# Kernel tuning notes

Hardware: AMD Instinct MI355X
Metric: run time of the kernel (lower is better)

Reference implementation:

```python
import jax, jax.numpy as jnp
import numpy as np

B, C, N, GP = 8, 512, 4096, 4


def _phi(x):
    return jax.nn.relu(x) + 1.0


def _ln(x, g, b):
    # LayerNorm over last dim, eps=1e-6 (matches nn.LayerNorm(C, eps=1e-6))
    mu = x.mean(-1, keepdims=True)
    var = ((x - mu) ** 2).mean(-1, keepdims=True)
    return (x - mu) * jax.lax.rsqrt(var + 1e-6) * g + b


def _sdpa_linear(q, k, v):
    # q,k,v: [G,C,n]
    c = q.shape[1]
    kv = jnp.einsum('gcn,gdn->gcd', k, v) / jnp.sqrt(jnp.asarray(c, q.dtype))
    ksum = k.sum(-1)                                              # [G,C]
    z = 1.0 / (jnp.einsum('gcn,gc->gn', q, ksum)[:, None, :] + 1e-6)  # [G,1,n]
    y = jnp.einsum('gcn,gcd->gdn', q, kv)                         # [G,C,n]
    return y * z


def _ffn_ln(x_res, y, g1, b1, f1w, f1b, f2w, f2b, g2, b2):
    # residual + ln1 + FFN + relu(ln2); io layout [G,C,n]
    h = _ln((x_res + y).transpose(0, 2, 1), g1, b1)               # [G,n,C]
    h = h + jnp.einsum('gnf,cf->gnc', jax.nn.relu(jnp.einsum('gnc,fc->gnf', h, f1w) + f1b), f2w) + f2b
    return jax.nn.relu(_ln(h, g2, b2)).transpose(0, 2, 1)


def _sa_block(x, wqk, wv, wphi, g1, b1, f1w, f1b, f2w, f2b, g2, b2):
    # SA_Layer_Linear: q_conv.weight == k_conv.weight, so q == k
    n = x.shape[-1]
    q = _phi(jnp.einsum('dc,gcn->gdn', wqk, x))
    v = jnp.einsum('dc,gcn->gdn', wv, x)
    phix = jnp.einsum('dc,gcn->gdn', wphi, x)
    qg = q.mean(-1, keepdims=True)                                # [G,C,1]
    alpha = jax.nn.softmax((qg * q).sum(1, keepdims=True), axis=-1) * n  # [G,1,n]
    y = _sdpa_linear(q, q * alpha, v) * phix
    return _ffn_ln(x, y, g1, b1, f1w, f1b, f2w, f2b, g2, b2)


def _cross_block(x, bsz, gp, wq, wk, wv, wphi, g1, b1, f1w, f1b, f2w, f2b, g2, b2):
    # Cross_SA_Layer_Linear: first group attends to k/v from group 0, rest passthrough
    n = x.shape[-1]
    first, rest = x[:bsz], x[bsz:]
    q = _phi(jnp.einsum('dc,gcn->gdn', wq, rest))                 # [(gp-1)B,C,n]
    k0 = _phi(jnp.einsum('dc,gcn->gdn', wk, first))               # [B,C,n]
    v0 = jnp.einsum('dc,gcn->gdn', wv, first)
    phi_first = jnp.einsum('dc,gcn->gdn', wphi, first)
    phi_rest = jnp.einsum('dc,gcn->gdn', wphi, rest)
    k = jnp.tile(k0, (gp - 1, 1, 1))
    v = jnp.tile(v0, (gp - 1, 1, 1))
    qg = jnp.tile(k0.mean(-1, keepdims=True), (gp - 1, 1, 1))
    alpha = jax.nn.softmax((qg * k).sum(1, keepdims=True), axis=-1) * n
    y = _sdpa_linear(q, k * alpha, v) * phi_rest                  # [(gp-1)B,C,n]
    y_first = y.mean(0, keepdims=True) * phi_first                # [B,C,n] via broadcast
    out_first = _ffn_ln(first, y_first, g1, b1, f1w, f1b, f2w, f2b, g2, b2)
    return jnp.concatenate([out_first, rest], axis=0)


def reference(feat, tw_qk, tw_v, tw_phi, tg1, tb1, tf1w, tf1b, tf2w, tf2b, tg2, tb2,
              cw_q, cw_k, cw_v, cw_phi, cg1, cb1, cf1w, cf1b, cf2w, cf2b, cg2, cb2):
    bsz, c, n = feat.shape
    gp = GP
    ng = n // gp
    # interval grouping: group i picks points {i, i+gp, i+2gp, ...}; vstack -> groups stacked on batch
    gx = (feat.transpose(0, 2, 1).reshape(bsz, ng, gp, c)
          .transpose(2, 0, 1, 3).reshape(gp * bsz, ng, c).transpose(0, 2, 1))
    f = _sa_block(gx, tw_qk, tw_v, tw_phi, tg1, tb1, tf1w, tf1b, tf2w, tf2b, tg2, tb2)
    # regroup: cat along feature dim then view(B,N,C) == interleave back
    t = (f.transpose(0, 2, 1).reshape(gp, bsz, ng, c)
         .transpose(1, 2, 0, 3).reshape(bsz, n, c))
    # contiguous re-split for cross block: group i = points [i*ng:(i+1)*ng]
    gx2 = (t.reshape(bsz, gp, ng, c).transpose(1, 0, 2, 3)
           .reshape(gp * bsz, ng, c).transpose(0, 2, 1))
    f2 = _cross_block(gx2, bsz, gp, cw_q, cw_k, cw_v, cw_phi, cg1, cb1, cf1w, cf1b, cf2w, cf2b, cg2, cb2)
    # final ungroup: out[i] = concat_j f2[B*j+i] -> [B,C,N]
    out = (f2.transpose(0, 2, 1).reshape(gp, bsz, ng, c)
           .transpose(1, 0, 2, 3).reshape(bsz, n, c).transpose(0, 2, 1))
    return out


def setup_inputs() -> dict:
    key = jax.random.key(0)
    ks = jax.random.split(key, 12)
    s = 0.02
    F = 4 * C
    d = {}
    d['feat'] = jax.random.normal(ks[0], (B, C, N), jnp.float32)
    # SA_Layer_Linear (trans_block) params
    d['tw_qk'] = jax.random.normal(ks[1], (C, C), jnp.float32) * s
    d['tw_v'] = jax.random.normal(ks[2], (C, C), jnp.float32) * s
    d['tw_phi'] = jax.random.normal(ks[3], (C, C), jnp.float32) * s
    d['tg1'] = jnp.ones((C,), jnp.float32)
    d['tb1'] = jnp.zeros((C,), jnp.float32)
    d['tf1w'] = jax.random.normal(ks[4], (F, C), jnp.float32) * s
    d['tf1b'] = jnp.zeros((F,), jnp.float32)
    d['tf2w'] = jax.random.normal(ks[5], (C, F), jnp.float32) * s
    d['tf2b'] = jnp.zeros((C,), jnp.float32)
    d['tg2'] = jnp.ones((C,), jnp.float32)
    d['tb2'] = jnp.zeros((C,), jnp.float32)
    # Cross_SA_Layer_Linear params
    d['cw_q'] = jax.random.normal(ks[6], (C, C), jnp.float32) * s
    d['cw_k'] = jax.random.normal(ks[7], (C, C), jnp.float32) * s
    d['cw_v'] = jax.random.normal(ks[8], (C, C), jnp.float32) * s
    d['cw_phi'] = jax.random.normal(ks[9], (C, C), jnp.float32) * s
    d['cg1'] = jnp.ones((C,), jnp.float32)
    d['cb1'] = jnp.zeros((C,), jnp.float32)
    d['cf1w'] = jax.random.normal(ks[10], (F, C), jnp.float32) * s
    d['cf1b'] = jnp.zeros((F,), jnp.float32)
    d['cf2w'] = jax.random.normal(ks[11], (C, F), jnp.float32) * s
    d['cf2b'] = jnp.zeros((C,), jnp.float32)
    d['cg2'] = jnp.ones((C,), jnp.float32)
    d['cb2'] = jnp.zeros((C,), jnp.float32)
    return d
```

## Files before the change

### kernel.cpp

```cpp
#include <hip/hip_runtime.h>
#include <math.h>

using u16 = unsigned short;
typedef __attribute__((ext_vector_type(8))) short short8;
typedef __attribute__((ext_vector_type(4))) float f32x4;

constexpr long kPLANE = 1024l * 512;
constexpr long SZW    = 512l * 512;
constexpr long MB     = 1l << 20;

__device__ __forceinline__ float bf2f(u16 u) {
  return __uint_as_float(((unsigned int)u) << 16);
}
__device__ __forceinline__ u16 f2bf(float f) {
  unsigned int x = __float_as_uint(f);
  x += 0x7fffu + ((x >> 16) & 1u);
  return (u16)(x >> 16);
}

__device__ __forceinline__ void lds_barrier() {
  asm volatile("s_waitcnt lgkmcnt(0)" ::: "memory");
  __builtin_amdgcn_s_barrier();
}

__global__ __launch_bounds__(256, 4) void gemm_mfma(
    const u16* __restrict__ A, long sA, int amask,
    const u16* __restrict__ B, long sB, int bmask,
    u16* __restrict__ Out, long sO,
    int M, int Nn, int K, float scale, int act,
    const float* __restrict__ bias,
    const float* __restrict__ rowscale, long sRS,
    const u16* __restrict__ pmul, const u16* __restrict__ resid)
{
  int gx = gridDim.x, gy = gridDim.y;
  int nwg = gx * gy * gridDim.z;
  int lin = blockIdx.x + gx * (blockIdx.y + gy * blockIdx.z);
  int qq = nwg >> 3, rr = nwg & 7;
  int xcd = lin & 7, idx = lin >> 3;
  int wg = (xcd < rr ? xcd * (qq + 1) : rr * (qq + 1) + (xcd - rr) * qq) + idx;
  int bx = wg % gx; int t_ = wg / gx; int by = t_ % gy; int g = t_ / gy;

  const u16* Ag = A + (long)(g & amask) * sA;
  const u16* Bg = B + (long)(g & bmask) * sB;
  u16* Og = Out + (long)g * sO;
  int m0 = by * 128, n0 = bx * 128;

  __shared__ __align__(16) u16 As[2][128 * 32];
  __shared__ __align__(16) u16 Bs[2][128 * 32];

  int tid = threadIdx.x;
  int w = tid >> 6, L = tid & 63;
  int wm = (w >> 1) * 64, wn = (w & 1) * 64;
  int l15 = L & 15, l4 = L >> 4;

  f32x4 acc[4][4] = {};

  int r0 = tid >> 2, r1 = r0 + 64;
  int kk = (tid & 3) * 8;
  int cxor = (tid >> 3) & 3;
  int s0 = r0 * 32 + (((tid & 3) ^ cxor) << 3);
  int s1 = s0 + 64 * 32;
  const u16* gA0 = Ag + (long)(m0 + r0) * K + kk;
  const u16* gA1 = Ag + (long)(m0 + r1) * K + kk;
  const u16* gB0 = Bg + (long)(n0 + r0) * K + kk;
  const u16* gB1 = Bg + (long)(n0 + r1) * K + kk;

  int rcol = (l4 << 3) ^ (((l15 >> 1) & 3) << 3);

  short8 ra0 = *(const short8*)gA0;
  short8 ra1 = *(const short8*)gA1;
  short8 rb0 = *(const short8*)gB0;
  short8 rb1 = *(const short8*)gB1;
  *(short8*)&As[0][s0] = ra0; *(short8*)&As[0][s1] = ra1;
  *(short8*)&Bs[0][s0] = rb0; *(short8*)&Bs[0][s1] = rb1;
  lds_barrier();

  int nsteps = K >> 5;
  for (int ks = 0; ks < nsteps; ++ks) {
    int cur = ks & 1;
    if (ks + 1 < nsteps) {
      int ko = (ks + 1) << 5;
      ra0 = *(const short8*)(gA0 + ko);
      ra1 = *(const short8*)(gA1 + ko);
      rb0 = *(const short8*)(gB0 + ko);
      rb1 = *(const short8*)(gB1 + ko);
    }
    short8 af[4], bf[4];
#pragma unroll
    for (int mi = 0; mi < 4; ++mi)
      af[mi] = *(const short8*)&As[cur][(wm + mi * 16 + l15) * 32 + rcol];
#pragma unroll
    for (int ni = 0; ni < 4; ++ni)
      bf[ni] = *(const short8*)&Bs[cur][(wn + ni * 16 + l15) * 32 + rcol];
#pragma unroll
    for (int mi = 0; mi < 4; ++mi)
#pragma unroll
      for (int ni = 0; ni < 4; ++ni)
        acc[mi][ni] = __builtin_amdgcn_mfma_f32_16x16x32_bf16(bf[ni], af[mi], acc[mi][ni], 0, 0, 0);
    if (ks + 1 < nsteps) {
      int nxt = cur ^ 1;
      *(short8*)&As[nxt][s0] = ra0; *(short8*)&As[nxt][s1] = ra1;
      *(short8*)&Bs[nxt][s0] = rb0; *(short8*)&Bs[nxt][s1] = rb1;
    }
    lds_barrier();
  }

#pragma unroll
  for (int mi = 0; mi < 4; ++mi) {
    int m = m0 + wm + mi * 16 + l15;
    float rs = rowscale ? rowscale[(long)g * sRS + m] : 1.f;
    float srs = scale * rs;
#pragma unroll
    for (int ni = 0; ni < 4; ++ni) {
      int nb = n0 + wn + ni * 16 + l4 * 4;
      long off = (long)m * Nn + nb;
      float v[4];
#pragma unroll
      for (int r = 0; r < 4; ++r) v[r] = acc[mi][ni][r] * srs;
      if (pmul) {
        ushort4 pm = *(const ushort4*)&pmul[(long)g * sO + off];
        v[0] *= bf2f(pm.x); v[1] *= bf2f(pm.y); v[2] *= bf2f(pm.z); v[3] *= bf2f(pm.w);
      }
      if (bias) {
        float4 bi = *(const float4*)&bias[nb];
        v[0] += bi.x; v[1] += bi.y; v[2] += bi.z; v[3] += bi.w;
      }
      if (resid) {
        ushort4 rd = *(const ushort4*)&resid[(long)g * sO + off];
        v[0] += bf2f(rd.x); v[1] += bf2f(rd.y); v[2] += bf2f(rd.z); v[3] += bf2f(rd.w);
      }
      if (act == 1) {
#pragma unroll
        for (int r = 0; r < 4; ++r) v[r] = fmaxf(v[r], 0.f);
      } else if (act == 2) {
#pragma unroll
        for (int r = 0; r < 4; ++r) v[r] = fmaxf(v[r], 0.f) + 1.f;
      }
      ushort4 o; o.x = f2bf(v[0]); o.y = f2bf(v[1]); o.z = f2bf(v[2]); o.w = f2bf(v[3]);
      *(ushort4*)&Og[off] = o;
    }
  }
}

__global__ __launch_bounds__(256) void cast7(
    const float* a0, const float* a1, const float* a2, const float* a3,
    const float* a4, const float* a5, const float* a6, u16* __restrict__ dst)
{
  int w = blockIdx.y;
  const float* s = w == 0 ? a0 : w == 1 ? a1 : w == 2 ? a2 : w == 3 ? a3
                 : w == 4 ? a4 : w == 5 ? a5 : a6;
  long i = (long)blockIdx.x * 256 + threadIdx.x;
  dst[(long)w * SZW + i] = f2bf(s[i]);
}

__global__ __launch_bounds__(256) void cast4(
    const float* a0, const float* a1, const float* a2, const float* a3,
    u16* __restrict__ dst)
{
  int w = blockIdx.y;
  const float* s = w == 0 ? a0 : w == 1 ? a1 : w == 2 ? a2 : a3;
  long i = (long)blockIdx.x * 256 + threadIdx.x;
  dst[(long)w * 1048576 + i] = f2bf(s[i]);
}

__global__ __launch_bounds__(256) void gather_feat(
    const float* __restrict__ feat, u16* __restrict__ gxT)
{
  __shared__ float t[32][132];
  int b = blockIdx.z, c0 = blockIdx.y * 32, nf0 = blockIdx.x * 128;
  int tx = threadIdx.x, ty = threadIdx.y;
  for (int r = ty; r < 32; r += 8)
    *(float4*)&t[r][tx * 4] = *(const float4*)&feat[((long)b * 512 + c0 + r) * 4096 + nf0 + tx * 4];
  __syncthreads();
  int n0o = nf0 >> 2;
  for (int gp = 0; gp < 4; ++gp) {
    long gbase = (long)(gp * 8 + b) * kPLANE;
    for (int jr = ty; jr < 32; jr += 8)
      gxT[gbase + (long)(n0o + jr) * 512 + c0 + tx] = f2bf(t[tx][jr * 4 + gp]);
  }
}

__global__ __launch_bounds__(256) void transpose_b(
    const u16* __restrict__ in, u16* __restrict__ out, const float* __restrict__ alpha)
{
  int g = blockIdx.z;
  const u16* I = in + (long)g * kPLANE;
  u16* O = out + (long)g * kPLANE;
  __shared__ u16 t[64][66];
  int n0 = blockIdx.x * 64, c0 = blockIdx.y * 64;
  int tx = threadIdx.x, ty = threadIdx.y;
  for (int r = ty; r < 64; r += 8)
    *(ushort2*)&t[r][tx * 2] = *(const ushort2*)&I[(long)(n0 + r) * 512 + c0 + tx * 2];
  __syncthreads();
  float al0 = 1.f, al1 = 1.f;
  if (alpha) {
    al0 = alpha[(long)g * 1024 + n0 + tx * 2];
    al1 = alpha[(long)g * 1024 + n0 + tx * 2 + 1];
  }
  for (int r = ty; r < 64; r += 8) {
    ushort2 wv;
    wv.x = f2bf(bf2f(t[tx * 2][r]) * al0);
    wv.y = f2bf(bf2f(t[tx * 2 + 1][r]) * al1);
    *(ushort2*)&O[(long)(c0 + r) * 1024 + n0 + tx * 2] = wv;
  }
}

__global__ __launch_bounds__(256) void colsum1(
    const u16* __restrict__ X, long sX, const float* __restrict__ alpha,
    float* __restrict__ part)
{
  int g = blockIdx.z, ch = blockIdx.y;
  int c = blockIdx.x * 256 + threadIdx.x;
  const u16* Xg = X + (long)g * sX;
  int nb = ch * 128;
  float s = 0.f;
  for (int i = 0; i < 128; ++i) {
    int n = nb + i;
    s += bf2f(Xg[(long)n * 512 + c]) * (alpha ? alpha[(long)g * 1024 + n] : 1.f);
  }
  part[(long)(g * 8 + ch) * 512 + c] = s;
}

__global__ __launch_bounds__(256) void colsum2(
    const float* __restrict__ part, float* __restrict__ out, float scale)
{
  int g = blockIdx.y;
  int c = blockIdx.x * 256 + threadIdx.x;
  float s = 0.f;
#pragma unroll
  for (int ch = 0; ch < 8; ++ch) s += part[(long)(g * 8 + ch) * 512 + c];
  out[(long)g * 512 + c] = s * scale;
}

__global__ __launch_bounds__(256) void rowdot(
    const u16* __restrict__ X, long sX, const float* __restrict__ w, int wmask,
    float* __restrict__ out, int mode)
{
  int g = blockIdx.y;
  int n = blockIdx.x * 4 + (threadIdx.x >> 6);
  int L = threadIdx.x & 63;
  const u16* row = X + (long)g * sX + (long)n * 512;
  short8 xv = *(const short8*)&row[L * 8];
  const float* wg = w + (long)(g & wmask) * 512;
  float4 w0 = *(const float4*)&wg[L * 8];
  float4 w1 = *(const float4*)&wg[L * 8 + 4];
  float s = bf2f((u16)xv[0]) * w0.x + bf2f((u16)xv[1]) * w0.y +
            bf2f((u16)xv[2]) * w0.z + bf2f((u16)xv[3]) * w0.w +
            bf2f((u16)xv[4]) * w1.x + bf2f((u16)xv[5]) * w1.y +
            bf2f((u16)xv[6]) * w1.z + bf2f((u16)xv[7]) * w1.w;
#pragma unroll
  for (int off = 32; off >= 1; off >>= 1) s += __shfl_down(s, off);
  if (L == 0) out[(long)g * 1024 + n] = mode ? 1.f / (s + 1e-6f) : s;
}

__global__ __launch_bounds__(256) void softmax_row(
    const float* __restrict__ sc, float* __restrict__ out)
{
  int g = blockIdx.x, tid = threadIdx.x;
  const float* s = sc + (long)g * 1024;
  float* o = out + (long)g * 1024;
  __shared__ float red[256];
  float lm = -3.4e38f;
  for (int n = tid; n < 1024; n += 256) lm = fmaxf(lm, s[n]);
  red[tid] = lm; __syncthreads();
  for (int st = 128; st; st >>= 1) { if (tid < st) red[tid] = fmaxf(red[tid], red[tid + st]); __syncthreads(); }
  float mx = red[0]; __syncthreads();
  float ls = 0.f;
  for (int n = tid; n < 1024; n += 256) ls += __expf(s[n] - mx);
  red[tid] = ls; __syncthreads();
  for (int st = 128; st; st >>= 1) { if (tid < st) red[tid] += red[tid + st]; __syncthreads(); }
  float inv = 1024.f / red[0];
  for (int n = tid; n < 1024; n += 256) o[n] = __expf(s[n] - mx) * inv;
}

__global__ __launch_bounds__(256) void ln_rows(
    const u16* __restrict__ X, const float* __restrict__ gamma,
    const float* __restrict__ beta, u16* __restrict__ Out, int relu)
{
  long m = (long)blockIdx.x * 4 + (threadIdx.x >> 6);
  int L = threadIdx.x & 63;
  const u16* x = X + m * 512;
  u16* o = Out + m * 512;
  short8 xv = *(const short8*)&x[L * 8];
  float v[8];
#pragma unroll
  for (int j = 0; j < 8; ++j) v[j] = bf2f((u16)xv[j]);
  float s = v[0] + v[1] + v[2] + v[3] + v[4] + v[5] + v[6] + v[7];
#pragma unroll
  for (int off = 32; off >= 1; off >>= 1) s += __shfl_xor(s, off);
  float mu = s * (1.f / 512.f);
  float ss = 0.f;
#pragma unroll
  for (int j = 0; j < 8; ++j) { v[j] -= mu; ss += v[j] * v[j]; }
#pragma unroll
  for (int off = 32; off >= 1; off >>= 1) ss += __shfl_xor(ss, off);
  float rs = rsqrtf(ss * (1.f / 512.f) + 1e-6f);
  float4 g0 = *(const float4*)&gamma[L * 8];
  float4 g1 = *(const float4*)&gamma[L * 8 + 4];
  float4 b0 = *(const float4*)&beta[L * 8];
  float4 b1 = *(const float4*)&beta[L * 8 + 4];
  float ov[8];
  ov[0] = v[0] * rs * g0.x + b0.x; ov[1] = v[1] * rs * g0.y + b0.y;
  ov[2] = v[2] * rs * g0.z + b0.z; ov[3] = v[3] * rs * g0.w + b0.w;
  ov[4] = v[4] * rs * g1.x + b1.x; ov[5] = v[5] * rs * g1.y + b1.y;
  ov[6] = v[6] * rs * g1.z + b1.z; ov[7] = v[7] * rs * g1.w + b1.w;
  if (relu) {
#pragma unroll
    for (int j = 0; j < 8; ++j) ov[j] = fmaxf(ov[j], 0.f);
  }
  short8 r;
#pragma unroll
  for (int j = 0; j < 8; ++j) r[j] = (short)f2bf(ov[j]);
  *(short8*)&o[L * 8] = r;
}

__global__ __launch_bounds__(256) void ln_gather(
    const u16* __restrict__ X, const float* __restrict__ gamma,
    const float* __restrict__ beta, u16* __restrict__ Out)
{
  long bid = (long)blockIdx.x * 4 + (threadIdx.x >> 6);
  int L = threadIdx.x & 63;
  int g2 = (int)(bid >> 10), m = (int)(bid & 1023);
  long src = ((long)((m & 3) * 8 + (g2 & 7)) * 1024 + (g2 >> 3) * 256 + (m >> 2)) * 512;
  const u16* x = X + src;
  u16* o = Out + bid * 512;
  short8 xv = *(const short8*)&x[L * 8];
  float v[8];
#pragma unroll
  for (int j = 0; j < 8; ++j) v[j] = bf2f((u16)xv[j]);
  float s = v[0] + v[1] + v[2] + v[3] + v[4] + v[5] + v[6] + v[7];
#pragma unroll
  for (int off = 32; off >= 1; off >>= 1) s += __shfl_xor(s, off);
  float mu = s * (1.f / 512.f);
  float ss = 0.f;
#pragma unroll
  for (int j = 0; j < 8; ++j) { v[j] -= mu; ss += v[j] * v[j]; }
#pragma unroll
  for (int off = 32; off >= 1; off >>= 1) ss += __shfl_xor(ss, off);
  float rs = rsqrtf(ss * (1.f / 512.f) + 1e-6f);
  float4 g0 = *(const float4*)&gamma[L * 8];
  float4 g1 = *(const float4*)&gamma[L * 8 + 4];
  float4 b0 = *(const float4*)&beta[L * 8];
  float4 b1 = *(const float4*)&beta[L * 8 + 4];
  float ov[8];
  ov[0] = v[0] * rs * g0.x + b0.x; ov[1] = v[1] * rs * g0.y + b0.y;
  ov[2] = v[2] * rs * g0.z + b0.z; ov[3] = v[3] * rs * g0.w + b0.w;
  ov[4] = v[4] * rs * g1.x + b1.x; ov[5] = v[5] * rs * g1.y + b1.y;
  ov[6] = v[6] * rs * g1.z + b1.z; ov[7] = v[7] * rs * g1.w + b1.w;
  short8 r;
#pragma unroll
  for (int j = 0; j < 8; ++j) r[j] = (short)f2bf(fmaxf(ov[j], 0.f));
  *(short8*)&o[L * 8] = r;
}

__global__ __launch_bounds__(256) void ybar_k(
    const u16* __restrict__ Y, float* __restrict__ yb)
{
  long idx = ((long)blockIdx.x * 256 + threadIdx.x) * 2;
  float s0 = 0.f, s1 = 0.f;
#pragma unroll
  for (int g = 0; g < 24; ++g) {
    ushort2 u = *(const ushort2*)&Y[(long)g * kPLANE + idx];
    s0 += bf2f(u.x); s1 += bf2f(u.y);
  }
  float2 o; o.x = s0 * (1.f / 24.f); o.y = s1 * (1.f / 24.f);
  *(float2*)&yb[idx] = o;
}

__global__ __launch_bounds__(256) void hfirst_ln(
    const u16* __restrict__ gx2, const u16* __restrict__ phiF,
    const float* __restrict__ yb, const float* __restrict__ gamma,
    const float* __restrict__ beta, u16* __restrict__ Out)
{
  long m = (long)blockIdx.x * 4 + (threadIdx.x >> 6);
  int L = threadIdx.x & 63;
  long off = m * 512 + L * 8;
  long yoff = (m & 1023) * 512 + L * 8;
  short8 a8 = *(const short8*)&gx2[off];
  short8 f8 = *(const short8*)&phiF[off];
  float4 y0 = *(const float4*)&yb[yoff];
  float4 y1 = *(const float4*)&yb[yoff + 4];
  float v[8];
  v[0] = bf2f((u16)a8[0]) + y0.x * bf2f((u16)f8[0]);
  v[1] = bf2f((u16)a8[1]) + y0.y * bf2f((u16)f8[1]);
  v[2] = bf2f((u16)a8[2]) + y0.z * bf2f((u16)f8[2]);
  v[3] = bf2f((u16)a8[3]) + y0.w * bf2f((u16)f8[3]);
  v[4] = bf2f((u16)a8[4]) + y1.x * bf2f((u16)f8[4]);
  v[5] = bf2f((u16)a8[5]) + y1.y * bf2f((u16)f8[5]);
  v[6] = bf2f((u16)a8[6]) + y1.z * bf2f((u16)f8[6]);
  v[7] = bf2f((u16)a8[7]) + y1.w * bf2f((u16)f8[7]);
  float s = v[0] + v[1] + v[2] + v[3] + v[4] + v[5] + v[6] + v[7];
#pragma unroll
  for (int off2 = 32; off2 >= 1; off2 >>= 1) s += __shfl_xor(s, off2);
  float mu = s * (1.f / 512.f);
  float ss = 0.f;
#pragma unroll
  for (int j = 0; j < 8; ++j) { v[j] -= mu; ss += v[j] * v[j]; }
#pragma unroll
  for (int off2 = 32; off2 >= 1; off2 >>= 1) ss += __shfl_xor(ss, off2);
  float rs = rsqrtf(ss * (1.f / 512.f) + 1e-6f);
  float4 g0 = *(const float4*)&gamma[L * 8];
  float4 g1 = *(const float4*)&gamma[L * 8 + 4];
  float4 b0 = *(const float4*)&beta[L * 8];
  float4 b1 = *(const float4*)&beta[L * 8 + 4];
  float ov[8];
  ov[0] = v[0] * rs * g0.x + b0.x; ov[1] = v[1] * rs * g0.y + b0.y;
  ov[2] = v[2] * rs * g0.z + b0.z; ov[3] = v[3] * rs * g0.w + b0.w;
  ov[4] = v[4] * rs * g1.x + b1.x; ov[5] = v[5] * rs * g1.y + b1.y;
  ov[6] = v[6] * rs * g1.z + b1.z; ov[7] = v[7] * rs * g1.w + b1.w;
  short8 r;
#pragma unroll
  for (int j = 0; j < 8; ++j) r[j] = (short)f2bf(ov[j]);
  *(short8*)&Out[off] = r;
}

__global__ __launch_bounds__(256) void assemble_t(
    const u16* __restrict__ gx2T, const u16* __restrict__ crossT,
    float* __restrict__ out)
{
  int g2 = blockIdx.z, gp2 = g2 >> 3, b = g2 & 7;
  const u16* S = (gp2 == 0) ? crossT + (long)b * kPLANE : gx2T + (long)g2 * kPLANE;
  __shared__ u16 t[32][33];
  int m0 = blockIdx.x * 32, c0 = blockIdx.y * 32;
  int tx = threadIdx.x, ty = threadIdx.y;
  for (int r = ty; r < 32; r += 8) t[r][tx] = S[(long)(m0 + r) * 512 + c0 + tx];
  __syncthreads();
  for (int r = ty; r < 32; r += 8)
    out[((long)b * 512 + c0 + r) * 4096 + gp2 * 1024 + m0 + tx] = bf2f(t[tx][r]);
}

extern "C" void kernel_launch(void* const* d_in, const int* in_sizes, int n_in,
                              void* d_out, int out_size, void* d_ws, size_t ws_size,
                              hipStream_t stream)
{
  const float* feat = (const float*)d_in[0];
  const float* tg1 = (const float*)d_in[4];  const float* tb1 = (const float*)d_in[5];
  const float* tf1b = (const float*)d_in[7];
  const float* tf2b = (const float*)d_in[9];
  const float* tg2 = (const float*)d_in[10]; const float* tb2 = (const float*)d_in[11];
  const float* cg1 = (const float*)d_in[16]; const float* cb1 = (const float*)d_in[17];
  const float* cf1b = (const float*)d_in[19];
  const float* cf2b = (const float*)d_in[21];
  const float* cg2 = (const float*)d_in[22]; const float* cb2 = (const float*)d_in[23];

  char* wsb = (char*)d_ws;
  u16* WP = (u16*)wsb;
  u16* WF = (u16*)(wsb + 4 * MB);
  float* SM = (float*)(wsb + 12 * MB);
  float* QG = SM;
  float* SC = SM + 16384;
  float* AL = SM + 49152;
  float* KS = SM + 81920;
  float* Zb = SM + 98304;
  float* ZR = SM + 131072;
  float* YB = SM + 155648;
  float* PART = SM + 688128;
  u16* P2 = (u16*)(wsb + 16 * MB);
  u16* P3 = (u16*)(wsb + 48 * MB);
  u16* P4 = (u16*)(wsb + 80 * MB);

  char* ob = (char*)d_out;
  u16* KV  = (u16*)ob;
  u16* GXT = (u16*)(ob + 16 * MB);
  u16* HID = (u16*)ob;
  u16* KV2 = (u16*)(ob + 32 * MB);
  u16* PHF = (u16*)(ob + 36 * MB);
  u16* K0S = (u16*)(ob + 44 * MB);
  u16* V0S = (u16*)(ob + 52 * MB);

  u16 *WPqk = WP,           *WPv  = WP + SZW,     *WPphi = WP + 2 * SZW,
      *WPcq = WP + 3 * SZW, *WPck = WP + 4 * SZW, *WPcv  = WP + 5 * SZW,
      *WPcphi = WP + 6 * SZW;
  u16 *WF1 = WF, *WF2 = WF + 1048576, *WF3 = WF + 2097152, *WF4 = WF + 3145728;

  dim3 b256(256), bT(32, 8);
  const float rsc = 1.0f / sqrtf(512.0f);
  const long PL = kPLANE;

  cast7<<<dim3(1024, 7), b256, 0, stream>>>(
      (const float*)d_in[1], (const float*)d_in[2], (const float*)d_in[3],
      (const float*)d_in[12], (const float*)d_in[13], (const float*)d_in[14],
      (const float*)d_in[15], WP);
  cast4<<<dim3(4096, 4), b256, 0, stream>>>(
      (const float*)d_in[6], (const float*)d_in[8],
      (const float*)d_in[18], (const float*)d_in[20], WF);

  gather_feat<<<dim3(32, 16, 8), bT, 0, stream>>>(feat, GXT);
  gemm_mfma<<<dim3(4, 8, 32), b256, 0, stream>>>(GXT, PL, 31, WPqk, 0, 0, P2, PL,
      1024, 512, 512, 1.f, 2, nullptr, nullptr, 0, nullptr, nullptr);
  colsum1<<<dim3(2, 8, 32), b256, 0, stream>>>(P2, PL, nullptr, PART);
  colsum2<<<dim3(2, 32), b256, 0, stream>>>(PART, QG, 1.f / 1024.f);
  rowdot<<<dim3(256, 32), b256, 0, stream>>>(P2, PL, QG, 31, SC, 0);
  softmax_row<<<32, b256, 0, stream>>>(SC, AL);
  gemm_mfma<<<dim3(4, 8, 32), b256, 0, stream>>>(GXT, PL, 31, WPv, 0, 0, P3, PL,
      1024, 512, 512, 1.f, 0, nullptr, nullptr, 0, nullptr, nullptr);
  transpose_b<<<dim3(16, 8, 32), bT, 0, stream>>>(P3, P4, nullptr);
  transpose_b<<<dim3(16, 8, 32), bT, 0, stream>>>(P2, P3, AL);
  gemm_mfma<<<dim3(4, 4, 32), b256, 0, stream>>>(P4, PL, 31, P3, PL, 31, KV, SZW,
      512, 512, 1024, rsc, 0, nullptr, nullptr, 0, nullptr, nullptr);
  colsum1<<<dim3(2, 8, 32), b256, 0, stream>>>(P2, PL, AL, PART);
  colsum2<<<dim3(2, 32), b256, 0, stream>>>(PART, KS, 1.f);
  rowdot<<<dim3(256, 32), b256, 0, stream>>>(P2, PL, KS, 31, Zb, 1);
  gemm_mfma<<<dim3(4, 8, 32), b256, 0, stream>>>(GXT, PL, 31, WPphi, 0, 0, P4, PL,
      1024, 512, 512, 1.f, 0, nullptr, nullptr, 0, nullptr, nullptr);
  gemm_mfma<<<dim3(4, 8, 32), b256, 0, stream>>>(P2, PL, 31, KV, SZW, 31, P3, PL,
      1024, 512, 512, 1.f, 0, nullptr, Zb, 1024, P4, GXT);
  ln_rows<<<8192, b256, 0, stream>>>(P3, tg1, tb1, P2, 0);
  for (int ch = 0; ch < 2; ++ch) {
    const u16* Hc = P2 + (long)ch * 16 * PL;
    gemm_mfma<<<dim3(16, 128, 1), b256, 0, stream>>>(Hc, 0, 0, WF1, 0, 0, HID, 0,
        16384, 2048, 512, 1.f, 1, tf1b, nullptr, 0, nullptr, nullptr);
    gemm_mfma<<<dim3(4, 128, 1), b256, 0, stream>>>(HID, 0, 0, WF2, 0, 0,
        P3 + (long)ch * 16 * PL, 0, 16384, 512, 2048, 1.f, 0, tf2b, nullptr, 0, nullptr, Hc);
  }
  ln_gather<<<8192, b256, 0, stream>>>(P3, tg2, tb2, P4);

  gemm_mfma<<<dim3(4, 8, 24), b256, 0, stream>>>(P4 + 8 * PL, PL, 31, WPcq, 0, 0, P2, PL,
      1024, 512, 512, 1.f, 2, nullptr, nullptr, 0, nullptr, nullptr);
  gemm_mfma<<<dim3(4, 8, 24), b256, 0, stream>>>(P4 + 8 * PL, PL, 31, WPcphi, 0, 0, P3, PL,
      1024, 512, 512, 1.f, 0, nullptr, nullptr, 0, nullptr, nullptr);
  gemm_mfma<<<dim3(4, 8, 8), b256, 0, stream>>>(P4, PL, 31, WPck, 0, 0, P2 + 24 * PL, PL,
      1024, 512, 512, 1.f, 2, nullptr, nullptr, 0, nullptr, nullptr);
  gemm_mfma<<<dim3(4, 8, 8), b256, 0, stream>>>(P4, PL, 31, WPcv, 0, 0, P3 + 24 * PL, PL,
      1024, 512, 512, 1.f, 0, nullptr, nullptr, 0, nullptr, nullptr);
  gemm_mfma<<<dim3(4, 8, 8), b256, 0, stream>>>(P4, PL, 31, WPcphi, 0, 0, PHF, PL,
      1024, 512, 512, 1.f, 0, nullptr, nullptr, 0, nullptr, nullptr);
  colsum1<<<dim3(2, 8, 8), b256, 0, stream>>>(P2 + 24 * PL, PL, nullptr, PART);
  colsum2<<<dim3(2, 8), b256, 0, stream>>>(PART, QG, 1.f / 1024.f);
  rowdot<<<dim3(256, 8), b256, 0, stream>>>(P2 + 24 * PL, PL, QG, 7, SC, 0);
  softmax_row<<<8, b256, 0, stream>>>(SC, AL);
  transpose_b<<<dim3(16, 8, 8), bT, 0, stream>>>(P2 + 24 * PL, K0S, AL);
  transpose_b<<<dim3(16, 8, 8), bT, 0, stream>>>(P3 + 24 * PL, V0S, nullptr);
  gemm_mfma<<<dim3(4, 4, 8), b256, 0, stream>>>(V0S, PL, 31, K0S, PL, 31, KV2, SZW,
      512, 512, 1024, rsc, 0, nullptr, nullptr, 0, nullptr, nullptr);
  colsum1<<<dim3(2, 8, 8), b256, 0, stream>>>(P2 + 24 * PL, PL, AL, PART);
  colsum2<<<dim3(2, 8), b256, 0, stream>>>(PART, KS, 1.f);
  rowdot<<<dim3(256, 24), b256, 0, stream>>>(P2, PL, KS, 7, ZR, 1);
  gemm_mfma<<<dim3(4, 8, 24), b256, 0, stream>>>(P2, PL, 31, KV2, SZW, 7, P3, PL,
      1024, 512, 512, 1.f, 0, nullptr, ZR, 1024, P3, nullptr);
  ybar_k<<<1024, b256, 0, stream>>>(P3, YB);
  hfirst_ln<<<2048, b256, 0, stream>>>(P4, PHF, YB, cg1, cb1, P3 + 24 * PL);
  gemm_mfma<<<dim3(16, 64, 1), b256, 0, stream>>>(P3 + 24 * PL, 0, 0, WF3, 0, 0, HID, 0,
      8192, 2048, 512, 1.f, 1, cf1b, nullptr, 0, nullptr, nullptr);
  gemm_mfma<<<dim3(4, 64, 1), b256, 0, stream>>>(HID, 0, 0, WF4, 0, 0, P2 + 24 * PL, 0,
      8192, 512, 2048, 1.f, 0, cf2b, nullptr, 0, nullptr, P3 + 24 * PL);
  ln_rows<<<2048, b256, 0, stream>>>(P2 + 24 * PL, cg2, cb2, P3 + 24 * PL, 1);
  assemble_t<<<dim3(32, 16, 32), bT, 0, stream>>>(P4, P3 + 24 * PL, (float*)d_out);
}
```

Measured before the change: 929.7 us.

## Use direct global-to-LDS loads with triple-buffered GEMM pipeline

The GEMM main loop now loads tiles straight into LDS with global_load_lds instead of staging them through registers, and uses three LDS buffers with a two-step prefetch distance. The swizzle moves to the global read address so the fixed per-thread LDS destination keeps the same bank-conflict-free layout. This takes register pressure and VGPR-to-LDS store work off the loop and deepens latency hiding. In exchange it uses more LDS and lowers the launch-bounds occupancy hint from 4 to 3 waves per SIMD.

After: 1.024 ms. +10.2%, slower.

```diff
diff --git a/kernel.cpp b/kernel.cpp
--- a/kernel.cpp
+++ b/kernel.cpp
@@ -18,12 +18,13 @@
   return (u16)(x >> 16);
 }
 
-__device__ __forceinline__ void lds_barrier() {
-  asm volatile("s_waitcnt lgkmcnt(0)" ::: "memory");
-  __builtin_amdgcn_s_barrier();
-}
-
-__global__ __launch_bounds__(256, 4) void gemm_mfma(
+__device__ __forceinline__ void gld16(const u16* g, u16* l) {
+  __builtin_amdgcn_global_load_lds(
+      (const __attribute__((address_space(1))) unsigned int*)g,
+      (__attribute__((address_space(3))) unsigned int*)l, 16, 0, 0);
+}
+
+__global__ __launch_bounds__(256, 3) void gemm_mfma(
     const u16* __restrict__ A, long sA, int amask,
     const u16* __restrict__ B, long sB, int bmask,
     u16* __restrict__ Out, long sO,
@@ -45,8 +46,8 @@
   u16* Og = Out + (long)g * sO;
   int m0 = by * 128, n0 = bx * 128;
 
-  __shared__ __align__(16) u16 As[2][128 * 32];
-  __shared__ __align__(16) u16 Bs[2][128 * 32];
+  __shared__ __align__(16) u16 As[3][128 * 32];
+  __shared__ __align__(16) u16 Bs[3][128 * 32];
 
   int tid = threadIdx.x;
   int w = tid >> 6, L = tid & 63;
@@ -56,34 +57,31 @@
   f32x4 acc[4][4] = {};
 
   int r0 = tid >> 2, r1 = r0 + 64;
-  int kk = (tid & 3) * 8;
-  int cxor = (tid >> 3) & 3;
-  int s0 = r0 * 32 + (((tid & 3) ^ cxor) << 3);
-  int s1 = s0 + 64 * 32;
-  const u16* gA0 = Ag + (long)(m0 + r0) * K + kk;
-  const u16* gA1 = Ag + (long)(m0 + r1) * K + kk;
-  const u16* gB0 = Bg + (long)(n0 + r0) * K + kk;
-  const u16* gB1 = Bg + (long)(n0 + r1) * K + kk;
+  int scol = (((tid & 3) ^ ((tid >> 3) & 3))) * 8;
+  int d0 = tid * 8, d1 = tid * 8 + 2048;
+  const u16* gA0 = Ag + (long)(m0 + r0) * K + scol;
+  const u16* gA1 = Ag + (long)(m0 + r1) * K + scol;
+  const u16* gB0 = Bg + (long)(n0 + r0) * K + scol;
+  const u16* gB1 = Bg + (long)(n0 + r1) * K + scol;
 
   int rcol = (l4 << 3) ^ (((l15 >> 1) & 3) << 3);
 
-  short8 ra0 = *(const short8*)gA0;
-  short8 ra1 = *(const short8*)gA1;
-  short8 rb0 = *(const short8*)gB0;
-  short8 rb1 = *(const short8*)gB1;
-  *(short8*)&As[0][s0] = ra0; *(short8*)&As[0][s1] = ra1;
-  *(short8*)&Bs[0][s0] = rb0; *(short8*)&Bs[0][s1] = rb1;
-  lds_barrier();
-
   int nsteps = K >> 5;
+
+  gld16(gA0, &As[0][d0]); gld16(gA1, &As[0][d1]);
+  gld16(gB0, &Bs[0][d0]); gld16(gB1, &Bs[0][d1]);
+  gld16(gA0 + 32, &As[1][d0]); gld16(gA1 + 32, &As[1][d1]);
+  gld16(gB0 + 32, &Bs[1][d0]); gld16(gB1 + 32, &Bs[1][d1]);
+  asm volatile("s_waitcnt vmcnt(4)" ::: "memory");
+  __builtin_amdgcn_s_barrier();
+
   for (int ks = 0; ks < nsteps; ++ks) {
-    int cur = ks & 1;
-    if (ks + 1 < nsteps) {
-      int ko = (ks + 1) << 5;
-      ra0 = *(const short8*)(gA0 + ko);
-      ra1 = *(const short8*)(gA1 + ko);
-      rb0 = *(const short8*)(gB0 + ko);
-      rb1 = *(const short8*)(gB1 + ko);
+    int cur = ks % 3;
+    if (ks + 2 < nsteps) {
+      int nb = (ks + 2) % 3;
+      int ko = (ks + 2) << 5;
+      gld16(gA0 + ko, &As[nb][d0]); gld16(gA1 + ko, &As[nb][d1]);
+      gld16(gB0 + ko, &Bs[nb][d0]); gld16(gB1 + ko, &Bs[nb][d1]);
     }
     short8 af[4], bf[4];
 #pragma unroll
@@ -97,12 +95,12 @@
 #pragma unroll
       for (int ni = 0; ni < 4; ++ni)
         acc[mi][ni] = __builtin_amdgcn_mfma_f32_16x16x32_bf16(bf[ni], af[mi], acc[mi][ni], 0, 0, 0);
-    if (ks + 1 < nsteps) {
-      int nxt = cur ^ 1;
-      *(short8*)&As[nxt][s0] = ra0; *(short8*)&As[nxt][s1] = ra1;
-      *(short8*)&Bs[nxt][s0] = rb0; *(short8*)&Bs[nxt][s1] = rb1;
-    }
-    lds_barrier();
+    if (ks + 2 < nsteps)
+      asm volatile("s_waitcnt vmcnt(4)" ::: "memory");
+    else
+      asm volatile("s_waitcnt vmcnt(0)" ::: "memory");
+    asm volatile("s_waitcnt lgkmcnt(0)" ::: "memory");
+    __builtin_amdgcn_s_barrier();
   }
 
 #pragma unroll
```
